# Performance work log

Hardware: AMD Instinct MI355X
Metric: run time of the kernel (lower is better)

## Reference

```python
import jax, jax.numpy as jnp
import numpy as np

DESIRED_SIZE = 512.0
STRIDE = DESIRED_SIZE / 16.0  # Constants.desired_size / 16
EPS = 1e-7
IOU_SCALE = 2.0
DIOU_SCALE = 0.5
SL1_SCALE = 1.0
GOOD_MULT = 2.0
BAD_MULT = 1.5


def setup_inputs() -> dict:
    key = jax.random.key(0)
    k1, k2 = jax.random.split(key)
    pred_boxes = jax.random.normal(k1, (64, 3, 32, 32, 5), dtype=jnp.float32)
    # uniform in [0, desired_size); every row has positive sum => all boxes valid,
    # so filter_and_trim keeps exactly max_boxes=100 per batch (fixed-k topk)
    target_boxes = jax.random.uniform(k2, (64, 100, 4), dtype=jnp.float32) * DESIRED_SIZE
    return {"pred_boxes": pred_boxes, "target_boxes": target_boxes}


def _postprocess(pred):
    # pred: [B, A, H, W, 5] -> absolute (x, y, w, h), conf
    B, A, H, W, _ = pred.shape
    cx = jnp.arange(W, dtype=pred.dtype)[None, None, None, :]
    cy = jnp.arange(H, dtype=pred.dtype)[None, None, :, None]
    x = (jax.nn.sigmoid(pred[..., 0]) + cx) * STRIDE
    y = (jax.nn.sigmoid(pred[..., 1]) + cy) * STRIDE
    wh = jnp.exp(pred[..., 2:4]) * STRIDE
    conf = jax.nn.sigmoid(pred[..., 4])
    return jnp.stack([x, y, wh[..., 0], wh[..., 1]], axis=-1), conf


def _fix_box_coordinates(b, epsilon=1.0):
    x1 = jnp.minimum(b[..., 0], b[..., 2])
    y1 = jnp.minimum(b[..., 1], b[..., 3])
    x2 = jnp.maximum(b[..., 0], b[..., 2])
    y2 = jnp.maximum(b[..., 1], b[..., 3])
    x2 = jnp.where(x1 == x2, x1 + epsilon, x2)
    y2 = jnp.where(y1 == y2, y1 + epsilon, y2)
    return jnp.stack([x1, y1, x2, y2], axis=-1)


def _yolo_to_corners(b):
    xc, yc, w, h = b[..., 0], b[..., 1], b[..., 2], b[..., 3]
    return jnp.stack([xc - w / 2, yc - h / 2, xc + w / 2, yc + h / 2], axis=-1)


def _box_iou(a, b):
    # torchvision.ops.box_iou: a [N,4], b [M,4] -> [N,M]
    area_a = (a[:, 2] - a[:, 0]) * (a[:, 3] - a[:, 1])
    area_b = (b[:, 2] - b[:, 0]) * (b[:, 3] - b[:, 1])
    lt = jnp.maximum(a[:, None, :2], b[None, :, :2])
    rb = jnp.minimum(a[:, None, 2:], b[None, :, 2:])
    wh = jnp.clip(rb - lt, 0.0)
    inter = wh[..., 0] * wh[..., 1]
    return inter / (area_a[:, None] + area_b[None, :] - inter)


def _diou_loss(p, t, eps=EPS):
    pa = jnp.clip(p[..., 2] - p[..., 0], 0.0) * jnp.clip(p[..., 3] - p[..., 1], 0.0)
    ta = jnp.clip(t[..., 2] - t[..., 0], 0.0) * jnp.clip(t[..., 3] - t[..., 1], 0.0)
    ix1 = jnp.maximum(p[..., 0], t[..., 0]); iy1 = jnp.maximum(p[..., 1], t[..., 1])
    ix2 = jnp.minimum(p[..., 2], t[..., 2]); iy2 = jnp.minimum(p[..., 3], t[..., 3])
    inter = jnp.clip(ix2 - ix1, 0.0) * jnp.clip(iy2 - iy1, 0.0)
    iou = inter / (pa + ta - inter + eps)
    pcx = (p[..., 0] + p[..., 2]) / 2; pcy = (p[..., 1] + p[..., 3]) / 2
    tcx = (t[..., 0] + t[..., 2]) / 2; tcy = (t[..., 1] + t[..., 3]) / 2
    cdist = (pcx - tcx) ** 2 + (pcy - tcy) ** 2
    ex1 = jnp.minimum(p[..., 0], t[..., 0]); ey1 = jnp.minimum(p[..., 1], t[..., 1])
    ex2 = jnp.maximum(p[..., 2], t[..., 2]); ey2 = jnp.maximum(p[..., 3], t[..., 3])
    diag = (ex2 - ex1) ** 2 + (ey2 - ey1) ** 2
    return 1.0 - (iou - cdist / (diag + eps))


def _smooth_l1_mean(p, t):
    d = p - t
    ad = jnp.abs(d)
    return jnp.mean(jnp.where(ad < 1.0, 0.5 * d * d, ad - 0.5))


def reference(pred_boxes, target_boxes):
    # negative-size penalty computed on RAW (pre-postprocess) width/height
    pw = pred_boxes[..., 2]
    ph = pred_boxes[..., 3]
    neg_pen = (jnp.clip(1.0 - pw, 0.0) + jnp.clip(1.0 - ph, 0.0)).mean()

    coords, conf = _postprocess(pred_boxes)
    B = pred_boxes.shape[0]
    coords = coords.reshape(B, -1, 4)   # [B, A*H*W, 4]
    conf = conf.reshape(B, -1)          # [B, A*H*W]

    K = target_boxes.shape[1]  # all targets valid by construction -> fixed k
    topv, topi = jax.lax.top_k(conf, K)                      # [B, K]
    pred_sel = jnp.take_along_axis(coords, topi[..., None], axis=1)  # [B, K, 4]

    target_flat = target_boxes.reshape(-1, 4)   # [N, 4], N = B*K
    pred_flat = pred_sel.reshape(-1, 4)
    conf_flat = topv.reshape(-1, 1)             # [N, 1]

    target_c = _fix_box_coordinates(target_flat)
    pred_c = _yolo_to_corners(pred_flat)

    # IoULoss: max over preds of full NxN IoU matrix, per target
    iou_mat = _box_iou(pred_c, target_c)
    max_iou = jnp.clip(jnp.nan_to_num(jnp.max(iou_mat, axis=0)), 0.0)
    iou_loss = 1.0 - max_iou                    # [N]

    sl1 = _smooth_l1_mean(pred_c, target_c) / DESIRED_SIZE  # scalar
    diou = _diou_loss(pred_c, target_c)         # [N]

    max_loss = IOU_SCALE + DIOU_SCALE + SL1_SCALE  # 3.5
    # NOTE: source adds UNSCALED diou into x (faithful to original)
    x = iou_loss * IOU_SCALE + diou + sl1 * SL1_SCALE   # [N]
    y = conf_flat                                        # [N, 1] -> broadcast to [N, N]
    good = jnp.sqrt((0.0 - x) ** 2 + (1.0 - y) ** 2) * GOOD_MULT
    bad = jnp.sqrt((max_loss - x) ** 2 + (1.0 - y) ** 2) * BAD_MULT
    losses = jnp.clip(jnp.mean(good - bad) + max_loss * BAD_MULT, 0.0)
    return losses + neg_pen
```

## Files before the change

### kernel.cpp

```cpp
#include <hip/hip_runtime.h>
#include <cmath>

#define NKEY 3072
#define KSEL 100
#define PCHUNK 200

static __device__ __forceinline__ float sigf(float v) {
    return 1.0f / (1.0f + expf(-v));
}

static __device__ double block_reduce_sum(double v) {
    __shared__ double sh[4];
    __syncthreads();
    for (int off = 32; off > 0; off >>= 1) v += __shfl_down(v, off, 64);
    int lane = threadIdx.x & 63, wid = threadIdx.x >> 6;
    if (lane == 0) sh[wid] = v;
    __syncthreads();
    v = (threadIdx.x < 4) ? sh[threadIdx.x] : 0.0;
    if (wid == 0) {
        v += __shfl_down(v, 2, 64);
        v += __shfl_down(v, 1, 64);
    }
    return v;
}

__global__ __launch_bounds__(256) void k_topk(const float* __restrict__ pred,
                                              const float* __restrict__ tgt,
                                              float* __restrict__ predc,
                                              float* __restrict__ targc,
                                              float* __restrict__ confv,
                                              unsigned int* __restrict__ maxiou_bits,
                                              double* __restrict__ negp ) {
    const int b = blockIdx.x;
    const int t = threadIdx.x;

    __shared__ unsigned long long keys[NKEY];
    __shared__ unsigned int hist[256];
    __shared__ unsigned long long sel[KSEL];
    __shared__ unsigned long long tkey_sh;
    __shared__ unsigned int scnt;
    __shared__ int bdigit_sh;
    __shared__ int bk_sh;

    if (t < KSEL) {
        int n = b * KSEL + t;
        const float* tb = tgt + (size_t)n * 4;
        float a0 = tb[0], a1 = tb[1], a2 = tb[2], a3 = tb[3];
        float x1 = fminf(a0, a2), y1 = fminf(a1, a3);
        float x2 = fmaxf(a0, a2), y2 = fmaxf(a1, a3);
        if (x1 == x2) x2 = x1 + 1.0f;
        if (y1 == y2) y2 = y1 + 1.0f;
        targc[n * 4 + 0] = x1; targc[n * 4 + 1] = y1;
        targc[n * 4 + 2] = x2; targc[n * 4 + 3] = y2;
        maxiou_bits[n] = 0u;
    }
    if (t == 0) scnt = 0;

    const float* pb = pred + (size_t)b * (NKEY * 5);
    float negacc = 0.0f;
    for (int r = 0; r < 12; ++r) {
        int idx = t + r * 256;
        const float* pe = pb + (size_t)idx * 5;
        float w = pe[2], h = pe[3], cl = pe[4];
        negacc += fmaxf(1.0f - w, 0.0f) + fmaxf(1.0f - h, 0.0f);
        float c = sigf(cl);
        keys[idx] = ((unsigned long long)__float_as_uint(c) << 32)
                  | (unsigned long long)(0xFFFFFFFFu - (unsigned)idx);
    }
    {
        double v = block_reduce_sum((double)negacc);
        if (t == 0) negp[b] = v;
    }
    __syncthreads();

    unsigned long long prefix = 0ull;
    int plen = 0;
    int k = KSEL;
    bool done = false;
    for (int round = 0; round < 8 && !done; ++round) {
        hist[t] = 0u;
        __syncthreads();
        int shift = 56 - 8 * round;
        for (int r = 0; r < 12; ++r) {
            unsigned long long key = keys[t + r * 256];
            if (plen == 0 || (key >> (64 - plen)) == (prefix >> (64 - plen))) {
                atomicAdd(&hist[(unsigned)((key >> shift) & 0xFFull)], 1u);
            }
        }
        __syncthreads();
        if (t < 64) {
            unsigned s0 = hist[4 * t + 0], s1 = hist[4 * t + 1];
            unsigned s2 = hist[4 * t + 2], s3 = hist[4 * t + 3];
            unsigned ssum = s0 + s1 + s2 + s3;
            unsigned suf = ssum;
            for (int off = 1; off < 64; off <<= 1) {
                unsigned o = __shfl_down(suf, off, 64);
                if (t + off < 64) suf += o;
            }
            unsigned above = suf - ssum;
            if (above < (unsigned)k && suf >= (unsigned)k) {
                unsigned hh[4] = {s0, s1, s2, s3};
                unsigned cum = above;
                for (int q = 3; q >= 0; --q) {
                    unsigned c = hh[q];
                    if (cum + c >= (unsigned)k) { bdigit_sh = 4 * t + q; bk_sh = k - (int)cum; break; }
                    cum += c;
                }
            }
        }
        __syncthreads();
        int d = bdigit_sh;
        k = bk_sh;
        prefix |= ((unsigned long long)(unsigned)d) << shift;
        plen += 8;
        unsigned ceq = hist[d];
        if (ceq == 1u) {
            for (int r = 0; r < 12; ++r) {
                unsigned long long key = keys[t + r * 256];
                if ((key >> (64 - plen)) == (prefix >> (64 - plen))) tkey_sh = key;
            }
            done = true;
        }
        __syncthreads();
    }
    unsigned long long T = tkey_sh;

    for (int r = 0; r < 12; ++r) {
        unsigned long long key = keys[t + r * 256];
        if (key >= T) {
            unsigned pos = atomicAdd(&scnt, 1u);
            sel[pos] = key;
        }
    }
    __syncthreads();
    if (t < KSEL) {
        unsigned long long key = sel[t];
        int rank = 0;
        for (int p = 0; p < KSEL; ++p) rank += (sel[p] > key) ? 1 : 0;
        unsigned idx = 0xFFFFFFFFu - (unsigned)(key & 0xFFFFFFFFull);
        float conf = __uint_as_float((unsigned)(key >> 32));
        int n = b * KSEL + rank;
        confv[n] = conf;
        const float* pe = pb + (size_t)idx * 5;
        int w = idx & 31, h = (idx >> 5) & 31;
        float x  = (sigf(pe[0]) + (float)w) * 32.0f;
        float y  = (sigf(pe[1]) + (float)h) * 32.0f;
        float bw = expf(pe[2]) * 32.0f;
        float bh = expf(pe[3]) * 32.0f;
        predc[n * 4 + 0] = x - bw * 0.5f;
        predc[n * 4 + 1] = y - bh * 0.5f;
        predc[n * 4 + 2] = x + bw * 0.5f;
        predc[n * 4 + 3] = y + bh * 0.5f;
    }
}

__global__ __launch_bounds__(256) void k_maxiou(const float* __restrict__ predc,
                                                const float* __restrict__ targc,
                                                unsigned int* __restrict__ maxiou_bits,
                                                float* __restrict__ diouv,
                                                double* __restrict__ sl1p ) {
    __shared__ float4 pl[PCHUNK];
    __shared__ float pa_sh[PCHUNK];
    int t = threadIdx.x;
    int j = blockIdx.x * 256 + t;
    const float4* pc4 = (const float4*)predc;
    int i0 = blockIdx.y * PCHUNK;
    for (int i = t; i < PCHUNK; i += 256) {
        float4 p = pc4[i0 + i];
        pl[i] = p;
        pa_sh[i] = (p.z - p.x) * (p.w - p.y);
    }
    float4 tj = ((const float4*)targc)[j];
    float ta = (tj.z - tj.x) * (tj.w - tj.y);
    __syncthreads();
    float m0 = 0.0f, m1 = 0.0f;
    #pragma unroll 2
    for (int i = 0; i < PCHUNK; i += 2) {
        float4 p = pl[i];
        float w0 = fmaxf(fminf(p.z, tj.z) - fmaxf(p.x, tj.x), 0.0f);
        float h0 = fmaxf(fminf(p.w, tj.w) - fmaxf(p.y, tj.y), 0.0f);
        float in0 = w0 * h0;
        float iou0 = in0 * __builtin_amdgcn_rcpf(pa_sh[i] + ta - in0);
        m0 = fmaxf(m0, iou0);
        float4 q = pl[i + 1];
        float w1 = fmaxf(fminf(q.z, tj.z) - fmaxf(q.x, tj.x), 0.0f);
        float h1 = fmaxf(fminf(q.w, tj.w) - fmaxf(q.y, tj.y), 0.0f);
        float in1 = w1 * h1;
        float iou1 = in1 * __builtin_amdgcn_rcpf(pa_sh[i + 1] + ta - in1);
        m1 = fmaxf(m1, iou1);
    }
    m0 = fmaxf(m0, m1);
    atomicMax(&maxiou_bits[j], __float_as_uint(m0));

    if (blockIdx.y == 0) {
        float4 p = pc4[j];
        float pa = fmaxf(p.z - p.x, 0.f) * fmaxf(p.w - p.y, 0.f);
        float ta2 = fmaxf(tj.z - tj.x, 0.f) * fmaxf(tj.w - tj.y, 0.f);
        float ix1 = fmaxf(p.x, tj.x), iy1 = fmaxf(p.y, tj.y);
        float ix2 = fminf(p.z, tj.z), iy2 = fminf(p.w, tj.w);
        float inter = fmaxf(ix2 - ix1, 0.f) * fmaxf(iy2 - iy1, 0.f);
        float iou = inter / (pa + ta2 - inter + 1e-7f);
        float pcx = (p.x + p.z) * 0.5f, pcy = (p.y + p.w) * 0.5f;
        float tcx = (tj.x + tj.z) * 0.5f, tcy = (tj.y + tj.w) * 0.5f;
        float cd = (pcx - tcx) * (pcx - tcx) + (pcy - tcy) * (pcy - tcy);
        float ex1 = fminf(p.x, tj.x), ey1 = fminf(p.y, tj.y);
        float ex2 = fmaxf(p.z, tj.z), ey2 = fmaxf(p.w, tj.w);
        float dg = (ex2 - ex1) * (ex2 - ex1) + (ey2 - ey1) * (ey2 - ey1);
        diouv[j] = 1.0f - (iou - cd / (dg + 1e-7f));
        double s = 0.0;
        {
            float d0 = p.x - tj.x, d1 = p.y - tj.y, d2 = p.z - tj.z, d3 = p.w - tj.w;
            float a0 = fabsf(d0), a1 = fabsf(d1), a2 = fabsf(d2), a3 = fabsf(d3);
            s += (double)(a0 < 1.f ? 0.5f * d0 * d0 : a0 - 0.5f);
            s += (double)(a1 < 1.f ? 0.5f * d1 * d1 : a1 - 0.5f);
            s += (double)(a2 < 1.f ? 0.5f * d2 * d2 : a2 - 0.5f);
            s += (double)(a3 < 1.f ? 0.5f * d3 * d3 : a3 - 0.5f);
        }
        double v = block_reduce_sum(s);
        if (t == 0) sl1p[blockIdx.x] = v;
    }
}

__global__ __launch_bounds__(256) void k_pair(const unsigned int* __restrict__ maxiou_bits,
                                              const float* __restrict__ diouv,
                                              const float* __restrict__ confv,
                                              const double* __restrict__ sl1p,
                                              double* __restrict__ pairp ) {
    __shared__ float oy2s[256];
    __shared__ float sl1_sh;
    int t = threadIdx.x;
    int j = blockIdx.x * 256 + t;
    if (t == 0) {
        double s = 0.0;
        for (int i = 0; i < 25; ++i) s += sl1p[i];
        sl1_sh = (float)(s / 25600.0 / 512.0);
    }
    {
        float oy = 1.0f - confv[blockIdx.y * 256 + t];
        oy2s[t] = oy * oy;
    }
    float mj = __uint_as_float(maxiou_bits[j]);
    float dj = diouv[j];
    __syncthreads();
    float xj = (1.0f - mj) * 2.0f + dj + sl1_sh;
    float a2 = xj * xj;
    float bb = 3.5f - xj;
    float b2 = bb * bb;
    float acc0 = 0.0f, acc1 = 0.0f;
    #pragma unroll 4
    for (int i = 0; i < 256; i += 2) {
        float o0 = oy2s[i], o1 = oy2s[i + 1];
        acc0 += 2.0f * __builtin_amdgcn_sqrtf(a2 + o0)
              - 1.5f * __builtin_amdgcn_sqrtf(b2 + o0);
        acc1 += 2.0f * __builtin_amdgcn_sqrtf(a2 + o1)
              - 1.5f * __builtin_amdgcn_sqrtf(b2 + o1);
    }
    double v = block_reduce_sum((double)(acc0 + acc1));
    if (t == 0) pairp[blockIdx.x * 25 + blockIdx.y] = v;
}

__global__ __launch_bounds__(256) void k_final(const double* __restrict__ pairp,
                                               const double* __restrict__ negp,
                                               float* __restrict__ out) {
    int t = threadIdx.x;
    double s = 0.0;
    for (int i = t; i < 625; i += 256) s += pairp[i];
    double ps = block_reduce_sum(s);
    double n = (t < 64) ? negp[t] : 0.0;
    double ns = block_reduce_sum(n);
    if (t == 0) {
        double mean_pair = ps / 40960000.0;
        float losses = fmaxf((float)mean_pair + 5.25f, 0.0f);
        float neg = (float)(ns / 196608.0);
        out[0] = losses + neg;
    }
}


extern "C" void kernel_launch(void* const* d_in, const int* in_sizes, int n_in,
                              void* d_out, int out_size, void* d_ws, size_t ws_size,
                              hipStream_t stream) {
    const float* pred = (const float*)d_in[0];
    const float* tgt  = (const float*)d_in[1];
    float* out = (float*)d_out;

    char* ws = (char*)d_ws;
    double* negp  = (double*)ws;
    double* sl1p  = negp + 64;
    double* pairp = negp + 96;
    float* fbase  = (float*)(ws + 6400);
    float* predc  = fbase;
    float* targc  = fbase + 25600;
    float* confv  = fbase + 51200;
    float* diouv  = fbase + 57600;
    unsigned int* maxiou_bits = (unsigned int*)(fbase + 64000);

    k_topk<<<64, 256, 0, stream>>>(pred, tgt, predc, targc, confv, maxiou_bits, negp);
    k_maxiou<<<dim3(25, 32), 256, 0, stream>>>(predc, targc, maxiou_bits, diouv, sl1p);
    k_pair<<<dim3(25, 25), 256, 0, stream>>>(maxiou_bits, diouv, confv, sl1p, pairp);
    k_final<<<1, 256, 0, stream>>>(pairp, negp, out);
}
```

Baseline: 107.4 us.

## Widen top-k blocks, finer IoU/pair grids, fold final reduce into pair kernel

```diff
diff --git a/kernel.cpp b/kernel.cpp
--- a/kernel.cpp
+++ b/kernel.cpp
@@ -3,34 +3,41 @@
 
 #define NKEY 3072
 #define KSEL 100
-#define PCHUNK 200
+#define TTOP 512
+#define TITER (NKEY / TTOP)
+#define PCHUNK 128
+#define ICHUNK 128
+#define NPAIRBLK (25 * 50)
 
 static __device__ __forceinline__ float sigf(float v) {
     return 1.0f / (1.0f + expf(-v));
 }
 
+template <int NWAVE>
 static __device__ double block_reduce_sum(double v) {
-    __shared__ double sh[4];
+    __shared__ double sh[NWAVE];
     __syncthreads();
     for (int off = 32; off > 0; off >>= 1) v += __shfl_down(v, off, 64);
     int lane = threadIdx.x & 63, wid = threadIdx.x >> 6;
     if (lane == 0) sh[wid] = v;
     __syncthreads();
-    v = (threadIdx.x < 4) ? sh[threadIdx.x] : 0.0;
+    v = (threadIdx.x < NWAVE) ? sh[threadIdx.x] : 0.0;
     if (wid == 0) {
-        v += __shfl_down(v, 2, 64);
-        v += __shfl_down(v, 1, 64);
+        #pragma unroll
+        for (int off = NWAVE / 2; off > 0; off >>= 1) v += __shfl_down(v, off, 64);
     }
     return v;
 }
 
-__global__ __launch_bounds__(256) void k_topk(const float* __restrict__ pred,
-                                              const float* __restrict__ tgt,
-                                              float* __restrict__ predc,
-                                              float* __restrict__ targc,
-                                              float* __restrict__ confv,
-                                              unsigned int* __restrict__ maxiou_bits,
-                                              double* __restrict__ negp ) {
+__global__ __launch_bounds__(TTOP) void k_topk(const float* __restrict__ pred,
+                                               const float* __restrict__ tgt,
+                                               float* __restrict__ predc,
+                                               float* __restrict__ targc,
+                                               float* __restrict__ confv,
+                                               unsigned int* __restrict__ maxiou_bits,
+                                               double* __restrict__ negp ,
+                                               double* __restrict__ pairSum,
+                                               unsigned int* __restrict__ pcnt) {
     const int b = blockIdx.x;
     const int t = threadIdx.x;
 
@@ -41,6 +48,8 @@
     __shared__ unsigned int scnt;
     __shared__ int bdigit_sh;
     __shared__ int bk_sh;
+
+    if (b == 0 && t == 0) { *pairSum = 0.0; *pcnt = 0u; }
 
     if (t < KSEL) {
         int n = b * KSEL + t;
@@ -58,8 +67,8 @@
 
     const float* pb = pred + (size_t)b * (NKEY * 5);
     float negacc = 0.0f;
-    for (int r = 0; r < 12; ++r) {
-        int idx = t + r * 256;
+    for (int r = 0; r < TITER; ++r) {
+        int idx = t + r * TTOP;
         const float* pe = pb + (size_t)idx * 5;
         float w = pe[2], h = pe[3], cl = pe[4];
         negacc += fmaxf(1.0f - w, 0.0f) + fmaxf(1.0f - h, 0.0f);
@@ -68,7 +77,7 @@
                   | (unsigned long long)(0xFFFFFFFFu - (unsigned)idx);
     }
     {
-        double v = block_reduce_sum((double)negacc);
+        double v = block_reduce_sum<8>((double)negacc);
         if (t == 0) negp[b] = v;
     }
     __syncthreads();
@@ -78,11 +87,11 @@
     int k = KSEL;
     bool done = false;
     for (int round = 0; round < 8 && !done; ++round) {
-        hist[t] = 0u;
+        if (t < 256) hist[t] = 0u;
         __syncthreads();
         int shift = 56 - 8 * round;
-        for (int r = 0; r < 12; ++r) {
-            unsigned long long key = keys[t + r * 256];
+        for (int r = 0; r < TITER; ++r) {
+            unsigned long long key = keys[t + r * TTOP];
             if (plen == 0 || (key >> (64 - plen)) == (prefix >> (64 - plen))) {
                 atomicAdd(&hist[(unsigned)((key >> shift) & 0xFFull)], 1u);
             }
@@ -115,8 +124,8 @@
         plen += 8;
         unsigned ceq = hist[d];
         if (ceq == 1u) {
-            for (int r = 0; r < 12; ++r) {
-                unsigned long long key = keys[t + r * 256];
+            for (int r = 0; r < TITER; ++r) {
+                unsigned long long key = keys[t + r * TTOP];
                 if ((key >> (64 - plen)) == (prefix >> (64 - plen))) tkey_sh = key;
             }
             done = true;
@@ -125,8 +134,8 @@
     }
     unsigned long long T = tkey_sh;
 
-    for (int r = 0; r < 12; ++r) {
-        unsigned long long key = keys[t + r * 256];
+    for (int r = 0; r < TITER; ++r) {
+        unsigned long long key = keys[t + r * TTOP];
         if (key >= T) {
             unsigned pos = atomicAdd(&scnt, 1u);
             sel[pos] = key;
@@ -165,31 +174,47 @@
     int j = blockIdx.x * 256 + t;
     const float4* pc4 = (const float4*)predc;
     int i0 = blockIdx.y * PCHUNK;
-    for (int i = t; i < PCHUNK; i += 256) {
-        float4 p = pc4[i0 + i];
-        pl[i] = p;
-        pa_sh[i] = (p.z - p.x) * (p.w - p.y);
+    if (t < PCHUNK) {
+        float4 p = pc4[i0 + t];
+        pl[t] = p;
+        pa_sh[t] = (p.z - p.x) * (p.w - p.y);
     }
     float4 tj = ((const float4*)targc)[j];
     float ta = (tj.z - tj.x) * (tj.w - tj.y);
     __syncthreads();
-    float m0 = 0.0f, m1 = 0.0f;
+    float m0 = 0.0f, m1 = 0.0f, m2 = 0.0f, m3 = 0.0f;
     #pragma unroll 2
-    for (int i = 0; i < PCHUNK; i += 2) {
-        float4 p = pl[i];
-        float w0 = fmaxf(fminf(p.z, tj.z) - fmaxf(p.x, tj.x), 0.0f);
-        float h0 = fmaxf(fminf(p.w, tj.w) - fmaxf(p.y, tj.y), 0.0f);
-        float in0 = w0 * h0;
-        float iou0 = in0 * __builtin_amdgcn_rcpf(pa_sh[i] + ta - in0);
-        m0 = fmaxf(m0, iou0);
-        float4 q = pl[i + 1];
-        float w1 = fmaxf(fminf(q.z, tj.z) - fmaxf(q.x, tj.x), 0.0f);
-        float h1 = fmaxf(fminf(q.w, tj.w) - fmaxf(q.y, tj.y), 0.0f);
-        float in1 = w1 * h1;
-        float iou1 = in1 * __builtin_amdgcn_rcpf(pa_sh[i + 1] + ta - in1);
-        m1 = fmaxf(m1, iou1);
-    }
-    m0 = fmaxf(m0, m1);
+    for (int i = 0; i < PCHUNK; i += 4) {
+        {
+            float4 p = pl[i];
+            float w = fmaxf(fminf(p.z, tj.z) - fmaxf(p.x, tj.x), 0.0f);
+            float h = fmaxf(fminf(p.w, tj.w) - fmaxf(p.y, tj.y), 0.0f);
+            float in = w * h;
+            m0 = fmaxf(m0, in * __builtin_amdgcn_rcpf(pa_sh[i] + ta - in));
+        }
+        {
+            float4 p = pl[i + 1];
+            float w = fmaxf(fminf(p.z, tj.z) - fmaxf(p.x, tj.x), 0.0f);
+            float h = fmaxf(fminf(p.w, tj.w) - fmaxf(p.y, tj.y), 0.0f);
+            float in = w * h;
+            m1 = fmaxf(m1, in * __builtin_amdgcn_rcpf(pa_sh[i + 1] + ta - in));
+        }
+        {
+            float4 p = pl[i + 2];
+            float w = fmaxf(fminf(p.z, tj.z) - fmaxf(p.x, tj.x), 0.0f);
+            float h = fmaxf(fminf(p.w, tj.w) - fmaxf(p.y, tj.y), 0.0f);
+            float in = w * h;
+            m2 = fmaxf(m2, in * __builtin_amdgcn_rcpf(pa_sh[i + 2] + ta - in));
+        }
+        {
+            float4 p = pl[i + 3];
+            float w = fmaxf(fminf(p.z, tj.z) - fmaxf(p.x, tj.x), 0.0f);
+            float h = fmaxf(fminf(p.w, tj.w) - fmaxf(p.y, tj.y), 0.0f);
+            float in = w * h;
+            m3 = fmaxf(m3, in * __builtin_amdgcn_rcpf(pa_sh[i + 3] + ta - in));
+        }
+    }
+    m0 = fmaxf(fmaxf(m0, m1), fmaxf(m2, m3));
     atomicMax(&maxiou_bits[j], __float_as_uint(m0));
 
     if (blockIdx.y == 0) {
@@ -216,7 +241,7 @@
             s += (double)(a2 < 1.f ? 0.5f * d2 * d2 : a2 - 0.5f);
             s += (double)(a3 < 1.f ? 0.5f * d3 * d3 : a3 - 0.5f);
         }
-        double v = block_reduce_sum(s);
+        double v = block_reduce_sum<4>(s);
         if (t == 0) sl1p[blockIdx.x] = v;
     }
 }
@@ -225,9 +250,13 @@
                                               const float* __restrict__ diouv,
                                               const float* __restrict__ confv,
                                               const double* __restrict__ sl1p,
-                                              double* __restrict__ pairp ) {
-    __shared__ float oy2s[256];
+                                              const double* __restrict__ negp,
+                                              double* __restrict__ pairSum,
+                                              unsigned int* __restrict__ pcnt,
+                                              float* __restrict__ out) {
+    __shared__ float oy2s[ICHUNK];
     __shared__ float sl1_sh;
+    __shared__ unsigned int ticket_sh;
     int t = threadIdx.x;
     int j = blockIdx.x * 256 + t;
     if (t == 0) {
@@ -235,8 +264,8 @@
         for (int i = 0; i < 25; ++i) s += sl1p[i];
         sl1_sh = (float)(s / 25600.0 / 512.0);
     }
-    {
-        float oy = 1.0f - confv[blockIdx.y * 256 + t];
+    if (t < ICHUNK) {
+        float oy = 1.0f - confv[blockIdx.y * ICHUNK + t];
         oy2s[t] = oy * oy;
     }
     float mj = __uint_as_float(maxiou_bits[j]);
@@ -248,31 +277,31 @@
     float b2 = bb * bb;
     float acc0 = 0.0f, acc1 = 0.0f;
     #pragma unroll 4
-    for (int i = 0; i < 256; i += 2) {
+    for (int i = 0; i < ICHUNK; i += 2) {
         float o0 = oy2s[i], o1 = oy2s[i + 1];
         acc0 += 2.0f * __builtin_amdgcn_sqrtf(a2 + o0)
               - 1.5f * __builtin_amdgcn_sqrtf(b2 + o0);
         acc1 += 2.0f * __builtin_amdgcn_sqrtf(a2 + o1)
               - 1.5f * __builtin_amdgcn_sqrtf(b2 + o1);
     }
-    double v = block_reduce_sum((double)(acc0 + acc1));
-    if (t == 0) pairp[blockIdx.x * 25 + blockIdx.y] = v;
-}
-
-__global__ __launch_bounds__(256) void k_final(const double* __restrict__ pairp,
-                                               const double* __restrict__ negp,
-                                               float* __restrict__ out) {
-    int t = threadIdx.x;
-    double s = 0.0;
-    for (int i = t; i < 625; i += 256) s += pairp[i];
-    double ps = block_reduce_sum(s);
-    double n = (t < 64) ? negp[t] : 0.0;
-    double ns = block_reduce_sum(n);
+    double v = block_reduce_sum<4>((double)(acc0 + acc1));
     if (t == 0) {
-        double mean_pair = ps / 40960000.0;
-        float losses = fmaxf((float)mean_pair + 5.25f, 0.0f);
-        float neg = (float)(ns / 196608.0);
-        out[0] = losses + neg;
+        atomicAdd(pairSum, v);
+        __threadfence();
+        ticket_sh = atomicAdd(pcnt, 1u);
+    }
+    __syncthreads();
+    if (ticket_sh == (unsigned)(NPAIRBLK - 1)) {
+        __threadfence();
+        double n = (t < 64) ? negp[t] : 0.0;
+        double ns = block_reduce_sum<4>(n);
+        if (t == 0) {
+            double ps = atomicAdd(pairSum, 0.0);
+            double mean_pair = ps / 40960000.0;
+            float losses = fmaxf((float)mean_pair + 5.25f, 0.0f);
+            float neg = (float)(ns / 196608.0);
+            out[0] = losses + neg;
+        }
     }
 }
 
@@ -287,16 +316,19 @@
     char* ws = (char*)d_ws;
     double* negp  = (double*)ws;
     double* sl1p  = negp + 64;
-    double* pairp = negp + 96;
-    float* fbase  = (float*)(ws + 6400);
+    double* pairSum = negp + 96;
+    unsigned int* pcnt = (unsigned int*)(negp + 97);
+    float* fbase  = (float*)(ws + 1024);
     float* predc  = fbase;
     float* targc  = fbase + 25600;
     float* confv  = fbase + 51200;
     float* diouv  = fbase + 57600;
     unsigned int* maxiou_bits = (unsigned int*)(fbase + 64000);
 
-    k_topk<<<64, 256, 0, stream>>>(pred, tgt, predc, targc, confv, maxiou_bits, negp);
-    k_maxiou<<<dim3(25, 32), 256, 0, stream>>>(predc, targc, maxiou_bits, diouv, sl1p);
-    k_pair<<<dim3(25, 25), 256, 0, stream>>>(maxiou_bits, diouv, confv, sl1p, pairp);
-    k_final<<<1, 256, 0, stream>>>(pairp, negp, out);
-}
+    k_topk<<<64, TTOP, 0, stream>>>(pred, tgt, predc, targc, confv, maxiou_bits,
+                                    negp, pairSum, pcnt);
+    k_maxiou<<<dim3(25, 6400 / PCHUNK), 256, 0, stream>>>(predc, targc, maxiou_bits,
+                                                          diouv, sl1p);
+    k_pair<<<dim3(25, 6400 / ICHUNK), 256, 0, stream>>>(maxiou_bits, diouv, confv,
+                                                        sl1p, negp, pairSum, pcnt, out);
+}
```

Result: slower. 120.1 us (+11.8%).
